# Kernel optimization log

Measured on AMD Instinct MI355X. Metric: run time of the kernel, lower is better.

## Reference

```python
import jax, jax.numpy as jnp
import numpy as np

EPS = 1e-5

def gamma_layer_norm(x, gamma):
    # LayerNorm over last dim with learnable gamma only (no bias)
    mu = jnp.mean(x, axis=-1, keepdims=True)
    var = jnp.var(x, axis=-1, keepdims=True)
    return (x - mu) * jax.lax.rsqrt(var + EPS) * gamma

def setup_inputs() -> dict:
    key = jax.random.key(0)
    k1, k2, k3, k4 = jax.random.split(key, 4)
    b, n, dim = 8, 4096, 512
    heads, head_size = 8, 64
    hidden = heads * head_size  # 512
    x = jax.random.normal(k1, (b, n, dim), dtype=jnp.float32)
    # nn.Linear(dim, hidden*3, bias=False): weight [3*hidden, dim]
    w_qkv = jax.random.normal(k2, (3 * hidden, dim), dtype=jnp.float32) * (dim ** -0.5)
    # nn.Linear(hidden, dim, bias=False): weight [dim, hidden]
    w_out = jax.random.normal(k3, (dim, hidden), dtype=jnp.float32) * (hidden ** -0.5)
    gamma = 1.0 + 0.02 * jax.random.normal(k4, (dim,), dtype=jnp.float32)
    return {"x": x, "w_qkv": w_qkv, "w_out": w_out, "gamma": gamma}

def reference(x, w_qkv, w_out, gamma):
    b, n, dim = x.shape
    heads, head_size = 8, 64
    scale = head_size ** -0.5
    # norm=False -> Identity; no time conditioning
    qkv = jnp.einsum('bnd,hd->bnh', x, w_qkv)  # [b, n, 3*hidden]
    q, k, v = jnp.split(qkv, 3, axis=-1)
    def to_heads(t):
        return t.reshape(b, n, heads, head_size).transpose(0, 2, 1, 3)  # b h n d
    q, k, v = to_heads(q), to_heads(k), to_heads(v)
    q = jax.nn.softmax(q, axis=-1) * scale   # softmax over feature dim
    k = jax.nn.softmax(k, axis=-2)           # softmax over sequence dim
    context = jnp.einsum('bhnd,bhne->bhde', k, v)      # [b, h, d, e]
    out = jnp.einsum('bhde,bhnd->bhne', context, q)    # [b, h, n, e]
    out = out.transpose(0, 2, 1, 3).reshape(b, n, heads * head_size)
    out = jnp.einsum('bnh,dh->bnd', out, w_out)
    out = gamma_layer_norm(out, gamma)  # dropout inactive (p=0 / eval)
    return out
```

## Files before the change

kernel.cpp:

```cpp
#include <hip/hip_runtime.h>
#include <hip/hip_bf16.h>
#include <stdint.h>
#include <stddef.h>

typedef __bf16 bf16_t;
typedef __bf16 bf16x8 __attribute__((ext_vector_type(8)));
typedef float floatx4 __attribute__((ext_vector_type(4)));

#define DIM 512
#define SEQ 4096
#define BATCH 8

static __device__ __forceinline__ floatx4 mfma_bf16(bf16x8 a, bf16x8 b, floatx4 c) {
  return __builtin_amdgcn_mfma_f32_16x16x32_bf16(a, b, c, 0, 0, 0);
}

typedef __attribute__((address_space(1))) const void* gas_ptr;
typedef __attribute__((address_space(3))) void* las_ptr;
static __device__ __forceinline__ void gll16(const void* g, void* l) {
  __builtin_amdgcn_global_load_lds((gas_ptr)g, (las_ptr)l, 16, 0, 0);
}

__global__ __launch_bounds__(256) void k_cvt2(const float* __restrict__ w, bf16_t* __restrict__ wb,
                                              const float* __restrict__ x, bf16_t* __restrict__ xb,
                                              float* __restrict__ S) {
  int blk = blockIdx.x;
  if (blk == 8576) {
    float4 zv = {0.f, 0.f, 0.f, 0.f};
    ((float4*)S)[threadIdx.x * 4]     = zv;
    ((float4*)S)[threadIdx.x * 4 + 1] = zv;
    ((float4*)S)[threadIdx.x * 4 + 2] = zv;
    ((float4*)S)[threadIdx.x * 4 + 3] = zv;
    return;
  }
  const float* src;
  bf16_t* dst;
  if (blk < 384) { src = w; dst = wb; }
  else           { src = x; dst = xb; blk -= 384; }
  int i = (blk * 256 + threadIdx.x) * 8;
  float4 a = *(const float4*)&src[i];
  float4 b = *(const float4*)&src[i + 4];
  bf16x8 o;
  o[0] = (bf16_t)a.x; o[1] = (bf16_t)a.y; o[2] = (bf16_t)a.z; o[3] = (bf16_t)a.w;
  o[4] = (bf16_t)b.x; o[5] = (bf16_t)b.y; o[6] = (bf16_t)b.z; o[7] = (bf16_t)b.w;
  *(bf16x8*)&dst[i] = o;
}

__global__ __launch_bounds__(512, 2) void k_qkv(const bf16_t* __restrict__ Xb,
                                                const bf16_t* __restrict__ Wb,
                                                bf16_t* __restrict__ qs,
                                                bf16_t* __restrict__ ek,
                                                bf16_t* __restrict__ vb,
                                                float* __restrict__ S) {
  __shared__ __align__(16) bf16_t As[2][256 * 64];
  __shared__ __align__(16) bf16_t Bs[2][256 * 64];
  const int tid = threadIdx.x;
  const int lane = tid & 63;
  const int w = tid >> 6;
  const int wr = w >> 2, wc = w & 3;
  const int l15 = lane & 15, l4 = lane >> 4;
  const int bid = blockIdx.x;
  const int xcd = bid & 7, local = bid >> 3;
  const int m0 = (xcd * 16 + local / 6) * 256;
  const int n0 = (local % 6) * 256;

  int sr[4], su[4];
#pragma unroll
  for (int i = 0; i < 4; ++i) {
    int s = tid + i * 512;
    sr[i] = s >> 3;
    su[i] = ((s & 7) ^ (sr[i] & 7)) << 3;
  }

  floatx4 acc[8][4];
#pragma unroll
  for (int i = 0; i < 8; ++i)
#pragma unroll
    for (int j = 0; j < 4; ++j) acc[i][j] = (floatx4){0.f, 0.f, 0.f, 0.f};

#pragma unroll
  for (int i = 0; i < 4; ++i) {
    int s = tid + i * 512;
    gll16(Xb + (size_t)(m0 + sr[i]) * DIM + su[i], &As[0][s * 8]);
    gll16(Wb + (size_t)(n0 + sr[i]) * DIM + su[i], &Bs[0][s * 8]);
  }

  for (int t = 0; t < 8; ++t) {
    const int cur = t & 1;
    if (t < 7) {
      const int kt = (t + 1) * 64;
#pragma unroll
      for (int i = 0; i < 4; ++i) {
        int s = tid + i * 512;
        gll16(Xb + (size_t)(m0 + sr[i]) * DIM + kt + su[i], &As[cur ^ 1][s * 8]);
        gll16(Wb + (size_t)(n0 + sr[i]) * DIM + kt + su[i], &Bs[cur ^ 1][s * 8]);
      }
      asm volatile("s_waitcnt vmcnt(8)" ::: "memory");
    } else {
      asm volatile("s_waitcnt vmcnt(0)" ::: "memory");
    }
    __builtin_amdgcn_s_barrier();
    __builtin_amdgcn_sched_barrier(0);
    __builtin_amdgcn_s_setprio(1);
#pragma unroll
    for (int kk = 0; kk < 2; ++kk) {
      bf16x8 af[8], bfr[4];
#pragma unroll
      for (int f = 0; f < 8; ++f) {
        int ar = wr * 128 + f * 16 + l15;
        int ua = (kk * 4 + l4) ^ (ar & 7);
        af[f] = *(const bf16x8*)(&As[cur][ar * 64 + ua * 8]);
      }
#pragma unroll
      for (int f = 0; f < 4; ++f) {
        int br = wc * 64 + f * 16 + l15;
        int ub = (kk * 4 + l4) ^ (br & 7);
        bfr[f] = *(const bf16x8*)(&Bs[cur][br * 64 + ub * 8]);
      }
#pragma unroll
      for (int i = 0; i < 8; ++i)
#pragma unroll
        for (int j = 0; j < 4; ++j)
          acc[i][j] = mfma_bf16(af[i], bfr[j], acc[i][j]);
    }
    __builtin_amdgcn_s_setprio(0);
    __builtin_amdgcn_sched_barrier(0);
    __builtin_amdgcn_s_barrier();
  }

  const int colbase = n0 + wc * 64;
  if (n0 < 512) {
#pragma unroll
    for (int fm = 0; fm < 8; ++fm) {
#pragma unroll
      for (int r = 0; r < 4; ++r) {
        float v0 = acc[fm][0][r], v1 = acc[fm][1][r], v2 = acc[fm][2][r], v3 = acc[fm][3][r];
        float mx = fmaxf(fmaxf(v0, v1), fmaxf(v2, v3));
        mx = fmaxf(mx, __shfl_xor(mx, 1));
        mx = fmaxf(mx, __shfl_xor(mx, 2));
        mx = fmaxf(mx, __shfl_xor(mx, 4));
        mx = fmaxf(mx, __shfl_xor(mx, 8));
        float e0 = __expf(v0 - mx), e1 = __expf(v1 - mx), e2 = __expf(v2 - mx), e3 = __expf(v3 - mx);
        float s = e0 + e1 + e2 + e3;
        s += __shfl_xor(s, 1); s += __shfl_xor(s, 2); s += __shfl_xor(s, 4); s += __shfl_xor(s, 8);
        float inv = 0.125f / s;
        int m = m0 + wr * 128 + fm * 16 + l4 * 4 + r;
        bf16_t* rowp = qs + (size_t)m * DIM + colbase;
        rowp[l15]      = (bf16_t)(e0 * inv);
        rowp[16 + l15] = (bf16_t)(e1 * inv);
        rowp[32 + l15] = (bf16_t)(e2 * inv);
        rowp[48 + l15] = (bf16_t)(e3 * inv);
      }
    }
  } else if (n0 < 1024) {
    const int cb = colbase - 512;
    float c0 = 0.f, c1 = 0.f, c2 = 0.f, c3 = 0.f;
#pragma unroll
    for (int fm = 0; fm < 8; ++fm) {
#pragma unroll
      for (int r = 0; r < 4; ++r) {
        int m = m0 + wr * 128 + fm * 16 + l4 * 4 + r;
        bf16_t* rowp = ek + (size_t)m * DIM + cb;
        float e0 = __expf(acc[fm][0][r]);
        float e1 = __expf(acc[fm][1][r]);
        float e2 = __expf(acc[fm][2][r]);
        float e3 = __expf(acc[fm][3][r]);
        rowp[l15]      = (bf16_t)e0;
        rowp[16 + l15] = (bf16_t)e1;
        rowp[32 + l15] = (bf16_t)e2;
        rowp[48 + l15] = (bf16_t)e3;
        c0 += e0; c1 += e1; c2 += e2; c3 += e3;
      }
    }
    c0 += __shfl_xor(c0, 16); c0 += __shfl_xor(c0, 32);
    c1 += __shfl_xor(c1, 16); c1 += __shfl_xor(c1, 32);
    c2 += __shfl_xor(c2, 16); c2 += __shfl_xor(c2, 32);
    c3 += __shfl_xor(c3, 16); c3 += __shfl_xor(c3, 32);
    if (lane < 16) {
      int b = m0 >> 12;
      atomicAdd(&S[b * 512 + cb + lane],      c0);
      atomicAdd(&S[b * 512 + cb + 16 + lane], c1);
      atomicAdd(&S[b * 512 + cb + 32 + lane], c2);
      atomicAdd(&S[b * 512 + cb + 48 + lane], c3);
    }
  } else {
    const int cb = colbase - 1024;
#pragma unroll
    for (int fm = 0; fm < 8; ++fm) {
#pragma unroll
      for (int r = 0; r < 4; ++r) {
        int m = m0 + wr * 128 + fm * 16 + l4 * 4 + r;
        bf16_t* rowp = vb + (size_t)m * DIM + cb;
        rowp[l15]      = (bf16_t)acc[fm][0][r];
        rowp[16 + l15] = (bf16_t)acc[fm][1][r];
        rowp[32 + l15] = (bf16_t)acc[fm][2][r];
        rowp[48 + l15] = (bf16_t)acc[fm][3][r];
      }
    }
  }
}

#define TP 136
__global__ __launch_bounds__(256) void k_ctx(const bf16_t* __restrict__ ek,
                                             const bf16_t* __restrict__ vb,
                                             float* __restrict__ ctxpart) {
  __shared__ __align__(16) bf16_t ekT[64 * TP];
  __shared__ __align__(16) bf16_t vT[64 * TP];
  __shared__ float red[4096];
  const int tid = threadIdx.x;
  const int lane = tid & 63, wid = tid >> 6;
  const int l15 = lane & 15, l4 = lane >> 4;
  const int bh = blockIdx.x, chunk = blockIdx.y;
  const int b = bh >> 3, h = bh & 7;
  const int base = b * SEQ + chunk * 512;

  floatx4 acc[4][4];
#pragma unroll
  for (int i = 0; i < 4; ++i)
#pragma unroll
    for (int j = 0; j < 4; ++j) acc[i][j] = (floatx4){0.f, 0.f, 0.f, 0.f};

  for (int nt = 0; nt < 4; ++nt) {
    const int n0 = base + nt * 128;
    if (nt) __syncthreads();
#pragma unroll
    for (int i = 0; i < 4; ++i) {
      int q = tid + i * 256;
      int n = q >> 3;
      int u = q & 7;
      bf16x8 vk = *(const bf16x8*)&ek[(size_t)(n0 + n) * DIM + h * 64 + u * 8];
      bf16x8 vv = *(const bf16x8*)&vb[(size_t)(n0 + n) * DIM + h * 64 + u * 8];
      int ncol = n ^ (u << 3);
#pragma unroll
      for (int j = 0; j < 8; ++j) {
        int c = u * 8 + j;
        ekT[c * TP + ncol] = vk[j];
        vT [c * TP + ncol] = vv[j];
      }
    }
    __syncthreads();
    const int nb = wid * 32;
    bf16x8 af[4], bfr[4];
#pragma unroll
    for (int f = 0; f < 4; ++f) {
      int c = f * 16 + l15;
      int colstart = (nb + l4 * 8) ^ (((c >> 3) & 7) << 3);
      af[f]  = *(const bf16x8*)&ekT[c * TP + colstart];
      bfr[f] = *(const bf16x8*)&vT [c * TP + colstart];
    }
#pragma unroll
    for (int i = 0; i < 4; ++i)
#pragma unroll
      for (int j = 0; j < 4; ++j)
        acc[i][j] = mfma_bf16(af[i], bfr[j], acc[i][j]);
  }

  __syncthreads();
  for (int w = 0; w < 4; ++w) {
    if (wid == w) {
#pragma unroll
      for (int fm = 0; fm < 4; ++fm)
#pragma unroll
        for (int fn = 0; fn < 4; ++fn)
#pragma unroll
          for (int r = 0; r < 4; ++r) {
            int d = fm * 16 + l4 * 4 + r;
            int e = fn * 16 + l15;
            if (w == 0) red[d * 64 + e] = acc[fm][fn][r];
            else        red[d * 64 + e] += acc[fm][fn][r];
          }
    }
    __syncthreads();
  }
  float* dst = ctxpart + ((size_t)bh * 8 + chunk) * 4096;
#pragma unroll
  for (int i = 0; i < 4; ++i) {
    int q = tid + i * 256;
    *(float4*)&dst[q * 4] = *(const float4*)&red[q * 4];
  }
}

__global__ __launch_bounds__(256) void k_mt(const float* __restrict__ ctxpart,
                                            const float* __restrict__ S,
                                            const float* __restrict__ w_out,
                                            bf16_t* __restrict__ Mt) {
  __shared__ float cs[4096];
  const int tid = threadIdx.x;
  const int bh = blockIdx.x;
  const int b = bh >> 3, h = bh & 7;
#pragma unroll
  for (int i = 0; i < 16; ++i) {
    int idx = tid + i * 256;
    float s = 0.f;
#pragma unroll
    for (int p = 0; p < 8; ++p) s += ctxpart[((size_t)bh * 8 + p) * 4096 + idx];
    cs[idx] = s / S[b * 512 + h * 64 + (idx >> 6)];
  }
  __syncthreads();
  for (int half = 0; half < 2; ++half) {
    const int dcol = half * 256 + tid;
    float a[64];
#pragma unroll
    for (int d = 0; d < 64; ++d) a[d] = 0.f;
    for (int e = 0; e < 64; ++e) {
      float we = w_out[(size_t)dcol * 512 + h * 64 + e];
#pragma unroll
      for (int d = 0; d < 64; ++d) a[d] += cs[d * 64 + e] * we;
    }
    bf16_t* dst = Mt + ((size_t)b * 512 + dcol) * 512 + h * 64;
#pragma unroll
    for (int g = 0; g < 8; ++g) {
      bf16x8 o;
#pragma unroll
      for (int j = 0; j < 8; ++j) o[j] = (bf16_t)a[g * 8 + j];
      *(bf16x8*)&dst[g * 8] = o;
    }
  }
}

__global__ __launch_bounds__(512, 2) void k_out(const bf16_t* __restrict__ qs,
                                                const bf16_t* __restrict__ Mt,
                                                const float* __restrict__ gamma,
                                                float* __restrict__ out) {
  __shared__ __align__(16) bf16_t As[2][128 * 64];
  __shared__ __align__(16) bf16_t Bs[512 * 64];
  __shared__ float redS[128 * 4];
  __shared__ float redQ[128 * 4];
  const int tid = threadIdx.x;
  const int lane = tid & 63;
  const int w = tid >> 6;
  const int wr = w >> 2, wc = w & 3;
  const int l15 = lane & 15, l4 = lane >> 4;
  const int bid = blockIdx.x;
  const int sbid = (bid & 7) * 32 + (bid >> 3);
  const int m0 = sbid * 128;
  const bf16_t* Bp = Mt + (size_t)(sbid >> 5) * 512 * 512;

  int aR[2], aU[2];
#pragma unroll
  for (int i = 0; i < 2; ++i) {
    int s = tid + i * 512;
    aR[i] = s >> 3;
    aU[i] = ((s & 7) ^ (aR[i] & 7)) << 3;
  }
  int bR[8], bU[8];
#pragma unroll
  for (int i = 0; i < 8; ++i) {
    int s = tid + i * 512;
    bR[i] = s >> 3;
    bU[i] = ((s & 7) ^ (bR[i] & 7)) << 3;
  }

  floatx4 acc[4][8];
#pragma unroll
  for (int i = 0; i < 4; ++i)
#pragma unroll
    for (int j = 0; j < 8; ++j) acc[i][j] = (floatx4){0.f, 0.f, 0.f, 0.f};

  bf16x8 breg[8];
#pragma unroll
  for (int i = 0; i < 2; ++i)
    gll16(qs + (size_t)(m0 + aR[i]) * 512 + aU[i], &As[0][(tid + i * 512) * 8]);
#pragma unroll
  for (int i = 0; i < 8; ++i)
    breg[i] = *(const bf16x8*)(Bp + (size_t)bR[i] * 512 + bU[i]);
  asm volatile("s_waitcnt vmcnt(0)" ::: "memory");
#pragma unroll
  for (int i = 0; i < 8; ++i)
    *(bf16x8*)(&Bs[(tid + i * 512) * 8]) = breg[i];
  asm volatile("s_waitcnt lgkmcnt(0)" ::: "memory");
  __builtin_amdgcn_s_barrier();

  for (int t = 0; t < 8; ++t) {
    const int cur = t & 1;
    if (t < 7) {
      const int kt = (t + 1) * 64;
#pragma unroll
      for (int i = 0; i < 2; ++i)
        gll16(qs + (size_t)(m0 + aR[i]) * 512 + kt + aU[i], &As[cur ^ 1][(tid + i * 512) * 8]);
#pragma unroll
      for (int i = 0; i < 8; ++i)
        breg[i] = *(const bf16x8*)(Bp + (size_t)bR[i] * 512 + kt + bU[i]);
    }
    __builtin_amdgcn_s_setprio(1);
#pragma unroll
    for (int kk = 0; kk < 2; ++kk) {
      bf16x8 af[4], bfr[8];
#pragma unroll
      for (int f = 0; f < 4; ++f) {
        int ar = wr * 64 + f * 16 + l15;
        int ua = (kk * 4 + l4) ^ (ar & 7);
        af[f] = *(const bf16x8*)(&As[cur][ar * 64 + ua * 8]);
      }
#pragma unroll
      for (int f = 0; f < 8; ++f) {
        int br = wc * 128 + f * 16 + l15;
        int ub = (kk * 4 + l4) ^ (br & 7);
        bfr[f] = *(const bf16x8*)(&Bs[br * 64 + ub * 8]);
      }
#pragma unroll
      for (int i = 0; i < 4; ++i)
#pragma unroll
        for (int j = 0; j < 8; ++j)
          acc[i][j] = mfma_bf16(af[i], bfr[j], acc[i][j]);
    }
    __builtin_amdgcn_s_setprio(0);
    __builtin_amdgcn_sched_barrier(0);
    __builtin_amdgcn_s_barrier();
    if (t < 7) {
      asm volatile("s_waitcnt vmcnt(0)" ::: "memory");
#pragma unroll
      for (int i = 0; i < 8; ++i)
        *(bf16x8*)(&Bs[(tid + i * 512) * 8]) = breg[i];
      asm volatile("s_waitcnt lgkmcnt(0)" ::: "memory");
      __builtin_amdgcn_s_barrier();
    }
  }

#pragma unroll
  for (int fm = 0; fm < 4; ++fm) {
#pragma unroll
    for (int r = 0; r < 4; ++r) {
      float s = 0.f, q = 0.f;
#pragma unroll
      for (int fn = 0; fn < 8; ++fn) {
        float v = acc[fm][fn][r];
        s += v; q += v * v;
      }
      s += __shfl_xor(s, 1); q += __shfl_xor(q, 1);
      s += __shfl_xor(s, 2); q += __shfl_xor(q, 2);
      s += __shfl_xor(s, 4); q += __shfl_xor(q, 4);
      s += __shfl_xor(s, 8); q += __shfl_xor(q, 8);
      if (l15 == 0) {
        int rl = wr * 64 + fm * 16 + l4 * 4 + r;
        redS[rl * 4 + wc] = s;
        redQ[rl * 4 + wc] = q;
      }
    }
  }
  __syncthreads();
  float gm[8];
#pragma unroll
  for (int fn = 0; fn < 8; ++fn) gm[fn] = gamma[wc * 128 + fn * 16 + l15];
#pragma unroll
  for (int fm = 0; fm < 4; ++fm) {
#pragma unroll
    for (int r = 0; r < 4; ++r) {
      int rl = wr * 64 + fm * 16 + l4 * 4 + r;
      float4 sv = *(const float4*)&redS[rl * 4];
      float4 qv = *(const float4*)&redQ[rl * 4];
      float Sr = sv.x + sv.y + sv.z + sv.w;
      float Qr = qv.x + qv.y + qv.z + qv.w;
      float mean = Sr * (1.f / 512.f);
      float var = Qr * (1.f / 512.f) - mean * mean;
      float rstd = rsqrtf(var + 1e-5f);
      float* rowp = out + (size_t)(m0 + rl) * 512 + wc * 128 + l15;
#pragma unroll
      for (int fn = 0; fn < 8; ++fn)
        rowp[fn * 16] = (acc[fm][fn][r] - mean) * rstd * gm[fn];
    }
  }
}

extern "C" void kernel_launch(void* const* d_in, const int* in_sizes, int n_in,
                              void* d_out, int out_size, void* d_ws, size_t ws_size,
                              hipStream_t stream) {
  const float* x     = (const float*)d_in[0];
  const float* w_qkv = (const float*)d_in[1];
  const float* w_out = (const float*)d_in[2];
  const float* gamma = (const float*)d_in[3];
  float* out = (float*)d_out;
  char* ws = (char*)d_ws;

  bf16_t* qs      = (bf16_t*)(ws);
  bf16_t* ek      = (bf16_t*)(ws + 33554432);
  bf16_t* vb      = (bf16_t*)(ws + 67108864);
  bf16_t* wqkvb   = (bf16_t*)(ws + 100663296);
  float*  S       = (float*)(ws + 102236160);
  bf16_t* Xb      = (bf16_t*)(ws + 102252544);
  float*  ctxpart = (float*)(ws + 103301120);
  bf16_t* Mt      = (bf16_t*)(ws + 111689728);

  k_cvt2<<<8577, 256, 0, stream>>>(w_qkv, wqkvb, x, Xb, S);

  k_qkv<<<768, 512, 0, stream>>>(Xb, wqkvb, qs, ek, vb, S);

  dim3 g2(64, 8);
  k_ctx<<<g2, 256, 0, stream>>>(ek, vb, ctxpart);

  k_mt<<<64, 256, 0, stream>>>(ctxpart, S, w_out, Mt);

  k_out<<<256, 512, 0, stream>>>(qs, Mt, gamma, out);
}
```

Before: 192.5 us.

## Shrink k_out tile to 64 rows with single-buffered direct-to-LDS loads

The output GEMM+LayerNorm kernel now uses 64-row tiles with 256 threads (4 waves) and launches 512 blocks instead of 256, with each wave covering all 64 rows of the tile. The double-buffered A tile and register-staged B loads are replaced by single-buffered global_load_lds for both operands, with a wait and barrier each k-step. This cuts LDS use so more blocks can fit per CU and removes the register staging. It gives up the overlap of loads with MFMA inside a block and reloads the B matrix twice as often per output row.

```diff
diff --git a/kernel.cpp b/kernel.cpp
--- a/kernel.cpp
+++ b/kernel.cpp
@@ -318,35 +318,34 @@
   }
 }
 
-__global__ __launch_bounds__(512, 2) void k_out(const bf16_t* __restrict__ qs,
+__global__ __launch_bounds__(256, 2) void k_out(const bf16_t* __restrict__ qs,
                                                 const bf16_t* __restrict__ Mt,
                                                 const float* __restrict__ gamma,
                                                 float* __restrict__ out) {
-  __shared__ __align__(16) bf16_t As[2][128 * 64];
+  __shared__ __align__(16) bf16_t As[64 * 64];
   __shared__ __align__(16) bf16_t Bs[512 * 64];
-  __shared__ float redS[128 * 4];
-  __shared__ float redQ[128 * 4];
+  __shared__ float redS[64 * 4];
+  __shared__ float redQ[64 * 4];
   const int tid = threadIdx.x;
   const int lane = tid & 63;
-  const int w = tid >> 6;
-  const int wr = w >> 2, wc = w & 3;
+  const int wc = tid >> 6;
   const int l15 = lane & 15, l4 = lane >> 4;
   const int bid = blockIdx.x;
-  const int sbid = (bid & 7) * 32 + (bid >> 3);
-  const int m0 = sbid * 128;
-  const bf16_t* Bp = Mt + (size_t)(sbid >> 5) * 512 * 512;
+  const int sbid = (bid & 7) * 64 + (bid >> 3);
+  const int m0 = sbid * 64;
+  const bf16_t* Bp = Mt + (size_t)(sbid >> 6) * 512 * 512;
 
   int aR[2], aU[2];
 #pragma unroll
   for (int i = 0; i < 2; ++i) {
-    int s = tid + i * 512;
+    int s = tid + i * 256;
     aR[i] = s >> 3;
     aU[i] = ((s & 7) ^ (aR[i] & 7)) << 3;
   }
-  int bR[8], bU[8];
-#pragma unroll
-  for (int i = 0; i < 8; ++i) {
-    int s = tid + i * 512;
+  int bR[16], bU[16];
+#pragma unroll
+  for (int i = 0; i < 16; ++i) {
+    int s = tid + i * 256;
     bR[i] = s >> 3;
     bU[i] = ((s & 7) ^ (bR[i] & 7)) << 3;
   }
@@ -357,40 +356,26 @@
 #pragma unroll
     for (int j = 0; j < 8; ++j) acc[i][j] = (floatx4){0.f, 0.f, 0.f, 0.f};
 
-  bf16x8 breg[8];
-#pragma unroll
-  for (int i = 0; i < 2; ++i)
-    gll16(qs + (size_t)(m0 + aR[i]) * 512 + aU[i], &As[0][(tid + i * 512) * 8]);
-#pragma unroll
-  for (int i = 0; i < 8; ++i)
-    breg[i] = *(const bf16x8*)(Bp + (size_t)bR[i] * 512 + bU[i]);
-  asm volatile("s_waitcnt vmcnt(0)" ::: "memory");
-#pragma unroll
-  for (int i = 0; i < 8; ++i)
-    *(bf16x8*)(&Bs[(tid + i * 512) * 8]) = breg[i];
-  asm volatile("s_waitcnt lgkmcnt(0)" ::: "memory");
-  __builtin_amdgcn_s_barrier();
-
   for (int t = 0; t < 8; ++t) {
-    const int cur = t & 1;
-    if (t < 7) {
-      const int kt = (t + 1) * 64;
-#pragma unroll
-      for (int i = 0; i < 2; ++i)
-        gll16(qs + (size_t)(m0 + aR[i]) * 512 + kt + aU[i], &As[cur ^ 1][(tid + i * 512) * 8]);
-#pragma unroll
-      for (int i = 0; i < 8; ++i)
-        breg[i] = *(const bf16x8*)(Bp + (size_t)bR[i] * 512 + kt + bU[i]);
-    }
+    const int kt = t * 64;
+    if (t) __builtin_amdgcn_s_barrier();
+#pragma unroll
+    for (int i = 0; i < 2; ++i)
+      gll16(qs + (size_t)(m0 + aR[i]) * 512 + kt + aU[i], &As[(tid + i * 256) * 8]);
+#pragma unroll
+    for (int i = 0; i < 16; ++i)
+      gll16(Bp + (size_t)bR[i] * 512 + kt + bU[i], &Bs[(tid + i * 256) * 8]);
+    asm volatile("s_waitcnt vmcnt(0)" ::: "memory");
+    __builtin_amdgcn_s_barrier();
     __builtin_amdgcn_s_setprio(1);
 #pragma unroll
     for (int kk = 0; kk < 2; ++kk) {
       bf16x8 af[4], bfr[8];
 #pragma unroll
       for (int f = 0; f < 4; ++f) {
-        int ar = wr * 64 + f * 16 + l15;
+        int ar = f * 16 + l15;
         int ua = (kk * 4 + l4) ^ (ar & 7);
-        af[f] = *(const bf16x8*)(&As[cur][ar * 64 + ua * 8]);
+        af[f] = *(const bf16x8*)(&As[ar * 64 + ua * 8]);
       }
 #pragma unroll
       for (int f = 0; f < 8; ++f) {
@@ -406,16 +391,8 @@
     }
     __builtin_amdgcn_s_setprio(0);
     __builtin_amdgcn_sched_barrier(0);
-    __builtin_amdgcn_s_barrier();
-    if (t < 7) {
-      asm volatile("s_waitcnt vmcnt(0)" ::: "memory");
-#pragma unroll
-      for (int i = 0; i < 8; ++i)
-        *(bf16x8*)(&Bs[(tid + i * 512) * 8]) = breg[i];
-      asm volatile("s_waitcnt lgkmcnt(0)" ::: "memory");
-      __builtin_amdgcn_s_barrier();
-    }
-  }
+  }
+  __builtin_amdgcn_s_barrier();
 
 #pragma unroll
   for (int fm = 0; fm < 4; ++fm) {
@@ -432,7 +409,7 @@
       s += __shfl_xor(s, 4); q += __shfl_xor(q, 4);
       s += __shfl_xor(s, 8); q += __shfl_xor(q, 8);
       if (l15 == 0) {
-        int rl = wr * 64 + fm * 16 + l4 * 4 + r;
+        int rl = fm * 16 + l4 * 4 + r;
         redS[rl * 4 + wc] = s;
         redQ[rl * 4 + wc] = q;
       }
@@ -446,7 +423,7 @@
   for (int fm = 0; fm < 4; ++fm) {
 #pragma unroll
     for (int r = 0; r < 4; ++r) {
-      int rl = wr * 64 + fm * 16 + l4 * 4 + r;
+      int rl = fm * 16 + l4 * 4 + r;
       float4 sv = *(const float4*)&redS[rl * 4];
       float4 qv = *(const float4*)&redQ[rl * 4];
       float Sr = sv.x + sv.y + sv.z + sv.w;
@@ -490,5 +467,5 @@
 
   k_mt<<<64, 256, 0, stream>>>(ctxpart, S, w_out, Mt);
 
-  k_out<<<256, 512, 0, stream>>>(qs, Mt, gamma, out);
-}
+  k_out<<<512, 256, 0, stream>>>(qs, Mt, gamma, out);
+}
```

Result: no change. 190.3 us, median of 2 (-1.1%).
